# Performance work log

Hardware: AMD Instinct MI355X
Metric: run time of the kernel (lower is better)

The kernel has to match this reference:

```python
import jax, jax.numpy as jnp
import numpy as np

B, S, HID = 1, 4096, 2048
NH, NKV, D = 16, 4, 128
BLK, M, K_TOP = 64, 32, 8
THETA = 10000.0
NEG = jnp.float32(-1e9)


def setup_inputs() -> dict:
    key = jax.random.key(0)
    ks = jax.random.split(key, 6)
    s = 0.02
    return {
        "hidden_states": jax.random.normal(ks[0], (B, S, HID), jnp.float32),
        "position_ids": jnp.arange(S, dtype=jnp.int32)[None, :],
        "Wq": jax.random.normal(ks[1], (HID, NH * D), jnp.float32) * s,
        "Wk": jax.random.normal(ks[2], (HID, NKV * D), jnp.float32) * s,
        "Wv": jax.random.normal(ks[3], (HID, NKV * D), jnp.float32) * s,
        "Wo": jax.random.normal(ks[4], (NH * D, HID), jnp.float32) * s,
        # seeded random-sign (Hadamard-style) sketch projection, non-trainable buffer
        "H_sketch": jnp.sign(jax.random.normal(ks[5], (D, M), jnp.float32)) / jnp.sqrt(jnp.float32(M)),
    }


def _rot_half(x):
    x1, x2 = x[..., : D // 2], x[..., D // 2 :]
    return jnp.concatenate([-x2, x1], axis=-1)


def reference(hidden_states, position_ids, Wq, Wk, Wv, Wo, H_sketch):
    # QKV projections -> [B, heads, S, D]
    q = (hidden_states @ Wq).reshape(B, S, NH, D).transpose(0, 2, 1, 3)
    k = (hidden_states @ Wk).reshape(B, S, NKV, D).transpose(0, 2, 1, 3)
    v = (hidden_states @ Wv).reshape(B, S, NKV, D).transpose(0, 2, 1, 3)

    # RoPE
    inv_freq = 1.0 / (THETA ** (jnp.arange(0, D, 2, dtype=jnp.float32) / D))
    freqs = position_ids.astype(jnp.float32)[:, :, None] * inv_freq[None, None, :]
    emb = jnp.concatenate([freqs, freqs], axis=-1)  # [B, S, D]
    cos, sin = jnp.cos(emb)[:, None], jnp.sin(emb)[:, None]  # [B, 1, S, D]
    q = q * cos + _rot_half(q) * sin
    k = k * cos + _rot_half(k) * sin

    # GQA repeat kv heads
    rep = NH // NKV
    k = jnp.repeat(k, rep, axis=1)
    v = jnp.repeat(v, rep, axis=1)

    nblk = S // BLK
    # Hadamard-sketch projections, block-mean pooled -> [B, NH, nblk, M]
    Sq = jnp.einsum("bhsd,dm->bhsm", q, H_sketch).reshape(B, NH, nblk, BLK, M).mean(axis=3)
    Sk = jnp.einsum("bhsd,dm->bhsm", k, H_sketch).reshape(B, NH, nblk, BLK, M).mean(axis=3)

    # Block-level sketch scores, causal at block granularity, diagonal forced in
    bs = jnp.einsum("bhim,bhjm->bhij", Sq, Sk)
    blk_causal = jnp.tril(jnp.ones((nblk, nblk), dtype=bool))
    bs = jnp.where(blk_causal, bs, NEG)
    bs = jnp.where(jnp.eye(nblk, dtype=bool), jnp.float32(1e9), bs)
    _, idx = jax.lax.top_k(bs, K_TOP)  # [B, NH, nblk, K_TOP]

    # Gather selected K/V blocks -> [B, NH, nblk, K_TOP, BLK, D]
    K5 = k.reshape(B, NH, nblk, BLK, D)
    V5 = v.reshape(B, NH, nblk, BLK, D)
    gidx = idx[..., None, None]
    Kg = jnp.take_along_axis(K5[:, :, None], gidx, axis=3)
    Vg = jnp.take_along_axis(V5[:, :, None], gidx, axis=3)

    # Block-sparse scores [B, NH, nblk, BLK, K_TOP, BLK]
    Qb = q.reshape(B, NH, nblk, BLK, D)
    scores = jnp.einsum("bhnqd,bhnkcd->bhnqkc", Qb, Kg) / jnp.sqrt(jnp.float32(D))

    # Token-level causal mask over gathered keys
    qpos = jnp.arange(nblk)[:, None] * BLK + jnp.arange(BLK)[None, :]  # [nblk, BLK]
    kpos = idx[..., None] * BLK + jnp.arange(BLK)  # [B, NH, nblk, K_TOP, BLK]
    mask = kpos[:, :, :, None] <= qpos[None, None, :, :, None, None]
    scores = jnp.where(mask, scores, NEG)

    probs = jax.nn.softmax(scores.reshape(B, NH, nblk, BLK, K_TOP * BLK), axis=-1)
    probs = probs.reshape(scores.shape)

    out = jnp.einsum("bhnqkc,bhnkcd->bhnqd", probs, Vg)
    out = out.reshape(B, NH, S, D).transpose(0, 2, 1, 3).reshape(B, S, NH * D)
    return out @ Wo
```

## Files before the change

### kernel.cpp

```cpp
#include <hip/hip_runtime.h>
#include <hip/hip_bf16.h>

#define S_LEN 4096
#define HID 2048
#define NH 16
#define NKV 4
#define HD 128
#define MSK 32
#define KTOP 8
#define NBLK 64
#define NEGV -1000000000.0f
#define SENT -3.0e38f

typedef __hip_bfloat16 bf16;
typedef __attribute__((ext_vector_type(8))) short short8;
typedef __attribute__((ext_vector_type(4))) float f32x4;


__device__ __forceinline__ unsigned short f2b(float v) {
    __hip_bfloat16 h = __float2bfloat16(v);
    return *reinterpret_cast<unsigned short*>(&h);
}
__device__ __forceinline__ float b2f(unsigned short u) {
    return __bfloat162float(*reinterpret_cast<__hip_bfloat16*>(&u));
}

__global__ __launch_bounds__(256) void splitT_W(
    const float* __restrict__ Wq, const float* __restrict__ Wk,
    const float* __restrict__ Wv, const float* __restrict__ Wo,
    bf16* __restrict__ WtqH, bf16* __restrict__ WtqL,
    bf16* __restrict__ WtkH, bf16* __restrict__ WtkL,
    bf16* __restrict__ WtvH, bf16* __restrict__ WtoH) {
    const int bx = blockIdx.x, k0 = blockIdx.y * 64;
    const float* W; unsigned short* TH; unsigned short* TL;
    int Nd, n0; bool hasLo;
    if (bx < 32)      { W = Wq; TH = (unsigned short*)WtqH; TL = (unsigned short*)WtqL; Nd = 2048; n0 = bx * 64; hasLo = true; }
    else if (bx < 40) { W = Wk; TH = (unsigned short*)WtkH; TL = (unsigned short*)WtkL; Nd = 512;  n0 = (bx - 32) * 64; hasLo = true; }
    else if (bx < 48) { W = Wv; TH = (unsigned short*)WtvH; TL = nullptr; Nd = 512;  n0 = (bx - 40) * 64; hasLo = false; }
    else              { W = Wo; TH = (unsigned short*)WtoH; TL = nullptr; Nd = 2048; n0 = (bx - 48) * 64; hasLo = false; }
    __shared__ float Ls[64][68];
    const int t = threadIdx.x;
    {
        const int kk = t >> 2, c0 = (t & 3) * 16;
#pragma unroll
        for (int i = 0; i < 4; i++)
            *(float4*)&Ls[kk][c0 + i * 4] =
                *(const float4*)&W[(size_t)(k0 + kk) * Nd + n0 + c0 + i * 4];
    }
    __syncthreads();
    const int c = t >> 2, ks = (t & 3) * 16;
    alignas(16) unsigned short hh[16];
    alignas(16) unsigned short ll[16];
#pragma unroll
    for (int j = 0; j < 16; j++) {
        const float x = Ls[ks + j][c];
        hh[j] = f2b(x);
        ll[j] = f2b(x - b2f(hh[j]));
    }
    const size_t db = (size_t)(n0 + c) * HID + k0 + ks;
    *(uint4*)&TH[db + 0] = *(const uint4*)&hh[0];
    *(uint4*)&TH[db + 8] = *(const uint4*)&hh[8];
    if (hasLo) {
        *(uint4*)&TL[db + 0] = *(const uint4*)&ll[0];
        *(uint4*)&TL[db + 8] = *(const uint4*)&ll[8];
    }
}

__global__ __launch_bounds__(256) void splitA(const float* __restrict__ A,
                                              bf16* __restrict__ Ahi,
                                              bf16* __restrict__ Alo) {
    const size_t i = ((size_t)blockIdx.x * 256 + threadIdx.x) * 4;
    const float4 v = *(const float4*)&A[i];
    ushort4 h, l;
    h.x = f2b(v.x); l.x = f2b(v.x - b2f(h.x));
    h.y = f2b(v.y); l.y = f2b(v.y - b2f(h.y));
    h.z = f2b(v.z); l.z = f2b(v.z - b2f(h.z));
    h.w = f2b(v.w); l.w = f2b(v.w - b2f(h.w));
    *(ushort4*)&((unsigned short*)Ahi)[i] = h;
    *(ushort4*)&((unsigned short*)Alo)[i] = l;
}

__global__ __launch_bounds__(256, 3) void proj3(
    const float* __restrict__ A,
    const bf16* __restrict__ Ahi_, const bf16* __restrict__ Alo_,
    const bf16* __restrict__ WtqH_, const bf16* __restrict__ WtqL_,
    const bf16* __restrict__ WtkH_, const bf16* __restrict__ WtkL_,
    const bf16* __restrict__ WtvH_,
    const int* __restrict__ pos_ids, const float* __restrict__ H,
    bf16* __restrict__ qf, bf16* __restrict__ kf, bf16* __restrict__ vfT,
    float* __restrict__ Sq, float* __restrict__ Sk) {
    const int u = blockIdx.x;
    const bool isQ = (u < 16);
    const bool isV = (u >= 20);
    const bool np3 = !isV;
    const int h = isQ ? u : (isV ? (u - 20) : (u - 16));
    const unsigned short* __restrict__ WH =
        (const unsigned short*)(isQ ? WtqH_ : (isV ? WtvH_ : WtkH_)) + (size_t)h * HD * HID;
    const unsigned short* __restrict__ WL =
        (const unsigned short*)(isQ ? WtqL_ : WtkL_) + (size_t)h * HD * HID;
    const unsigned short* __restrict__ AH = (const unsigned short*)Ahi_;
    const unsigned short* __restrict__ AL = (const unsigned short*)Alo_;
    bf16* __restrict__ Xout = isQ ? qf : kf;
    float* __restrict__ Sout = isQ ? Sq : Sk;
    const int Nd = isQ ? (NH * HD) : (NKV * HD);

    const int m0g = blockIdx.y * 128;
    const int t = threadIdx.x;
    const int w = t >> 6, L = t & 63;
    const int lm = L & 15, lq = L >> 4;

    __shared__ __align__(16) unsigned short shmem[4 * 128 * 40];
    __shared__ float red[4][128];
    unsigned short(*pAh)[40] = (unsigned short(*)[40])(shmem);
    unsigned short(*pAl)[40] = (unsigned short(*)[40])(shmem + 128 * 40);
    unsigned short(*pWh)[40] = (unsigned short(*)[40])(shmem + 2 * 128 * 40);
    unsigned short(*pWl)[40] = (unsigned short(*)[40])(shmem + 3 * 128 * 40);

    f32x4 acc[2][8];
#pragma unroll
    for (int mt = 0; mt < 2; mt++)
#pragma unroll
        for (int nt = 0; nt < 8; nt++) acc[mt][nt] = (f32x4){0.f, 0.f, 0.f, 0.f};

    const int hrow = t >> 1, hk0 = (t & 1) * 16;

    for (int k0 = 0; k0 < HID; k0 += 32) {
        __syncthreads();
        if (AH) {
            const unsigned short* sa = &AH[(size_t)(m0g + hrow) * HID + k0 + hk0];
            *(uint4*)&pAh[hrow][hk0 + 0] = *(const uint4*)&sa[0];
            *(uint4*)&pAh[hrow][hk0 + 8] = *(const uint4*)&sa[8];
            if (np3) {
                const unsigned short* sl = &AL[(size_t)(m0g + hrow) * HID + k0 + hk0];
                *(uint4*)&pAl[hrow][hk0 + 0] = *(const uint4*)&sl[0];
                *(uint4*)&pAl[hrow][hk0 + 8] = *(const uint4*)&sl[8];
            }
        } else {
#pragma unroll
            for (int i = 0; i < 4; i++) {
                const int idx = t + i * 256;
                const int row = idx >> 3, f4 = idx & 7;
                const float4 v = *(const float4*)&A[(size_t)(m0g + row) * HID + k0 + f4 * 4];
                ushort4 uh;
                uh.x = f2b(v.x); uh.y = f2b(v.y); uh.z = f2b(v.z); uh.w = f2b(v.w);
                *(ushort4*)&pAh[row][f4 * 4] = uh;
                if (np3) {
                    ushort4 ul;
                    ul.x = f2b(v.x - b2f(uh.x)); ul.y = f2b(v.y - b2f(uh.y));
                    ul.z = f2b(v.z - b2f(uh.z)); ul.w = f2b(v.w - b2f(uh.w));
                    *(ushort4*)&pAl[row][f4 * 4] = ul;
                }
            }
        }
        {
            const unsigned short* sh = &WH[(size_t)hrow * HID + k0 + hk0];
            *(uint4*)&pWh[hrow][hk0 + 0] = *(const uint4*)&sh[0];
            *(uint4*)&pWh[hrow][hk0 + 8] = *(const uint4*)&sh[8];
            if (np3) {
                const unsigned short* sl = &WL[(size_t)hrow * HID + k0 + hk0];
                *(uint4*)&pWl[hrow][hk0 + 0] = *(const uint4*)&sl[0];
                *(uint4*)&pWl[hrow][hk0 + 8] = *(const uint4*)&sl[8];
            }
        }
        __syncthreads();
        short8 ah[2], al[2];
#pragma unroll
        for (int mt = 0; mt < 2; mt++) {
            ah[mt] = *(const short8*)&pAh[w * 32 + mt * 16 + lm][lq * 8];
            if (np3) al[mt] = *(const short8*)&pAl[w * 32 + mt * 16 + lm][lq * 8];
        }
#pragma unroll
        for (int nt = 0; nt < 8; nt++) {
            const short8 bh = *(const short8*)&pWh[nt * 16 + lm][lq * 8];
#pragma unroll
            for (int mt = 0; mt < 2; mt++)
                acc[mt][nt] = __builtin_amdgcn_mfma_f32_16x16x32_bf16(ah[mt], bh, acc[mt][nt], 0, 0, 0);
            if (np3) {
                const short8 bl = *(const short8*)&pWl[nt * 16 + lm][lq * 8];
#pragma unroll
                for (int mt = 0; mt < 2; mt++) {
                    acc[mt][nt] = __builtin_amdgcn_mfma_f32_16x16x32_bf16(ah[mt], bl, acc[mt][nt], 0, 0, 0);
                    acc[mt][nt] = __builtin_amdgcn_mfma_f32_16x16x32_bf16(al[mt], bh, acc[mt][nt], 0, 0, 0);
                }
            }
        }
    }

    if (isV) {
        __syncthreads();
        unsigned short(*Tv)[136] = (unsigned short(*)[136])shmem;
#pragma unroll
        for (int mt = 0; mt < 2; mt++) {
            const int rb = w * 32 + mt * 16 + lq * 4;
#pragma unroll
            for (int rr = 0; rr < 4; rr++)
#pragma unroll
                for (int nt = 0; nt < 8; nt++)
                    Tv[nt * 16 + lm][rb + rr] = f2b(acc[mt][nt][rr]);
        }
        __syncthreads();
        const int col = t >> 1, rh = (t & 1) * 64;
        bf16* dst = &vfT[((size_t)h * HD + col) * S_LEN + m0g + rh];
#pragma unroll
        for (int u2 = 0; u2 < 8; u2++)
            *(uint4*)&dst[u2 * 8] = *(const uint4*)&Tv[col][rh + u2 * 8];
        return;
    }

    {
        float invf[4];
#pragma unroll
        for (int c4 = 0; c4 < 4; c4++) {
            const int jj = c4 * 16 + lm;
            invf[c4] = 1.0f / powf(10000.0f, (float)jj * (1.0f / 64.0f));
        }
#pragma unroll
        for (int mt = 0; mt < 2; mt++) {
            const int rbase = w * 32 + mt * 16 + lq * 4;
#pragma unroll
            for (int rr = 0; rr < 4; rr++) {
                const float p = (float)pos_ids[m0g + rbase + rr];
#pragma unroll
                for (int c4 = 0; c4 < 4; c4++) {
                    const float fr = p * invf[c4];
                    float sv, cv;
                    sincosf(fr, &sv, &cv);
                    const float x1 = acc[mt][c4][rr];
                    const float x2 = acc[mt][c4 + 4][rr];
                    acc[mt][c4][rr]     = x1 * cv - x2 * sv;
                    acc[mt][c4 + 4][rr] = x2 * cv + x1 * sv;
                }
            }
        }
    }

    float cs[8];
#pragma unroll
    for (int nt = 0; nt < 8; nt++) cs[nt] = 0.f;
#pragma unroll
    for (int mt = 0; mt < 2; mt++) {
        const int rbase = w * 32 + mt * 16 + lq * 4;
#pragma unroll
        for (int rr = 0; rr < 4; rr++) {
            bf16* dst = &Xout[(size_t)(m0g + rbase + rr) * Nd + h * HD + lm];
#pragma unroll
            for (int nt = 0; nt < 8; nt++) {
                const float v = acc[mt][nt][rr];
                dst[nt * 16] = __float2bfloat16(v);
                cs[nt] += v;
            }
        }
    }
#pragma unroll
    for (int nt = 0; nt < 8; nt++) {
        cs[nt] += __shfl_xor(cs[nt], 16);
        cs[nt] += __shfl_xor(cs[nt], 32);
    }
    if (lq == 0) {
#pragma unroll
        for (int nt = 0; nt < 8; nt++) red[w][nt * 16 + lm] = cs[nt];
    }
    __syncthreads();
    if (t < 64) {
        const int b = t >> 5, m = t & 31;
        float s = 0.f;
        for (int d = 0; d < 128; d++)
            s += (red[b * 2][d] + red[b * 2 + 1][d]) * H[d * MSK + m];
        Sout[((size_t)h * NBLK + (m0g >> 6) + b) * MSK + m] = s * (1.0f / 64.0f);
    }
}

__global__ __launch_bounds__(256, 3) void proj_rope_sketch(
    const float* __restrict__ A, const float* __restrict__ Wq,
    const float* __restrict__ Wk, const float* __restrict__ Wv,
    const int* __restrict__ pos_ids, const float* __restrict__ H,
    bf16* __restrict__ qf, bf16* __restrict__ kf, bf16* __restrict__ vf,
    float* __restrict__ Sq, float* __restrict__ Sk,
    int u0, int r0, int xbase) {
    const int u = blockIdx.x + u0;
    const bool isQ = (u < 16);
    const bool isV = (u >= 20);
    const bool np3 = !isV;
    const int h = isQ ? u : (isV ? (u - 20) : (u - 16));
    const float* __restrict__ W = isQ ? Wq : (isV ? Wv : Wk);
    const int Nd = isQ ? (NH * HD) : (NKV * HD);
    bf16* __restrict__ Xout = isQ ? qf : kf;
    float* __restrict__ Sout = isQ ? Sq : Sk;

    const int m0g = r0 + blockIdx.y * 128;
    const int m0x = isQ ? (m0g - xbase) : m0g;
    const int t = threadIdx.x;
    const int w = t >> 6, L = t & 63;
    const int lm = L & 15, lq = L >> 4;

    __shared__ __align__(16) unsigned short shmem[4 * 128 * 40];
    __shared__ float red[4][128];
    unsigned short(*pAh)[40] = (unsigned short(*)[40])(shmem);
    unsigned short(*pAl)[40] = (unsigned short(*)[40])(shmem + 128 * 40);
    unsigned short(*pWh)[40] = (unsigned short(*)[40])(shmem + 2 * 128 * 40);
    unsigned short(*pWl)[40] = (unsigned short(*)[40])(shmem + 3 * 128 * 40);

    f32x4 acc[2][8];
#pragma unroll
    for (int mt = 0; mt < 2; mt++)
#pragma unroll
        for (int nt = 0; nt < 8; nt++) acc[mt][nt] = (f32x4){0.f, 0.f, 0.f, 0.f};

    for (int k0 = 0; k0 < HID; k0 += 32) {
        __syncthreads();
#pragma unroll
        for (int i = 0; i < 4; i++) {
            const int idx = t + i * 256;
            const int row = idx >> 3, f4 = idx & 7;
            const float4 v = *(const float4*)&A[(size_t)(m0g + row) * HID + k0 + f4 * 4];
            ushort4 uh;
            uh.x = f2b(v.x); uh.y = f2b(v.y); uh.z = f2b(v.z); uh.w = f2b(v.w);
            *(ushort4*)&pAh[row][f4 * 4] = uh;
            if (np3) {
                ushort4 ul;
                ul.x = f2b(v.x - b2f(uh.x)); ul.y = f2b(v.y - b2f(uh.y));
                ul.z = f2b(v.z - b2f(uh.z)); ul.w = f2b(v.w - b2f(uh.w));
                *(ushort4*)&pAl[row][f4 * 4] = ul;
            }
        }
        {
            const int wcol = t >> 1, wk0 = (t & 1) * 16;
            const float* wp = &W[(size_t)(k0 + wk0) * Nd + h * HD + wcol];
            alignas(16) unsigned short hh[16];
            alignas(16) unsigned short ll[16];
#pragma unroll
            for (int uu = 0; uu < 16; uu++) {
                const float x = wp[(size_t)uu * Nd];
                hh[uu] = f2b(x);
                ll[uu] = f2b(x - b2f(hh[uu]));
            }
            *(uint4*)&pWh[wcol][wk0 + 0] = *(const uint4*)&hh[0];
            *(uint4*)&pWh[wcol][wk0 + 8] = *(const uint4*)&hh[8];
            if (np3) {
                *(uint4*)&pWl[wcol][wk0 + 0] = *(const uint4*)&ll[0];
                *(uint4*)&pWl[wcol][wk0 + 8] = *(const uint4*)&ll[8];
            }
        }
        __syncthreads();
        short8 ah[2], al[2];
#pragma unroll
        for (int mt = 0; mt < 2; mt++) {
            ah[mt] = *(const short8*)&pAh[w * 32 + mt * 16 + lm][lq * 8];
            if (np3) al[mt] = *(const short8*)&pAl[w * 32 + mt * 16 + lm][lq * 8];
        }
#pragma unroll
        for (int nt = 0; nt < 8; nt++) {
            const short8 bh = *(const short8*)&pWh[nt * 16 + lm][lq * 8];
#pragma unroll
            for (int mt = 0; mt < 2; mt++)
                acc[mt][nt] = __builtin_amdgcn_mfma_f32_16x16x32_bf16(ah[mt], bh, acc[mt][nt], 0, 0, 0);
            if (np3) {
                const short8 bl = *(const short8*)&pWl[nt * 16 + lm][lq * 8];
#pragma unroll
                for (int mt = 0; mt < 2; mt++) {
                    acc[mt][nt] = __builtin_amdgcn_mfma_f32_16x16x32_bf16(ah[mt], bl, acc[mt][nt], 0, 0, 0);
                    acc[mt][nt] = __builtin_amdgcn_mfma_f32_16x16x32_bf16(al[mt], bh, acc[mt][nt], 0, 0, 0);
                }
            }
        }
    }

    if (isV) {
        __syncthreads();
        unsigned short(*Tv)[136] = (unsigned short(*)[136])shmem;
#pragma unroll
        for (int mt = 0; mt < 2; mt++) {
            const int rb = w * 32 + mt * 16 + lq * 4;
#pragma unroll
            for (int rr = 0; rr < 4; rr++)
#pragma unroll
                for (int nt = 0; nt < 8; nt++)
                    Tv[nt * 16 + lm][rb + rr] = f2b(acc[mt][nt][rr]);
        }
        __syncthreads();
        const int col = t >> 1, rh = (t & 1) * 64;
        bf16* dst = &vf[((size_t)h * HD + col) * S_LEN + m0g + rh];
#pragma unroll
        for (int u2 = 0; u2 < 8; u2++)
            *(uint4*)&dst[u2 * 8] = *(const uint4*)&Tv[col][rh + u2 * 8];
        return;
    }

    {
        float invf[4];
#pragma unroll
        for (int c4 = 0; c4 < 4; c4++) {
            const int jj = c4 * 16 + lm;
            invf[c4] = 1.0f / powf(10000.0f, (float)jj * (1.0f / 64.0f));
        }
#pragma unroll
        for (int mt = 0; mt < 2; mt++) {
            const int rbase = w * 32 + mt * 16 + lq * 4;
#pragma unroll
            for (int rr = 0; rr < 4; rr++) {
                const float p = (float)pos_ids[m0g + rbase + rr];
#pragma unroll
                for (int c4 = 0; c4 < 4; c4++) {
                    const float fr = p * invf[c4];
                    float sv, cv;
                    sincosf(fr, &sv, &cv);
                    const float x1 = acc[mt][c4][rr];
                    const float x2 = acc[mt][c4 + 4][rr];
                    acc[mt][c4][rr]     = x1 * cv - x2 * sv;
                    acc[mt][c4 + 4][rr] = x2 * cv + x1 * sv;
                }
            }
        }
    }

    float cs[8];
#pragma unroll
    for (int nt = 0; nt < 8; nt++) cs[nt] = 0.f;
#pragma unroll
    for (int mt = 0; mt < 2; mt++) {
        const int rbase = w * 32 + mt * 16 + lq * 4;
#pragma unroll
        for (int rr = 0; rr < 4; rr++) {
            bf16* dst = &Xout[(size_t)(m0x + rbase + rr) * Nd + h * HD + lm];
#pragma unroll
            for (int nt = 0; nt < 8; nt++) {
                const float v = acc[mt][nt][rr];
                dst[nt * 16] = __float2bfloat16(v);
                cs[nt] += v;
            }
        }
    }
#pragma unroll
    for (int nt = 0; nt < 8; nt++) {
        cs[nt] += __shfl_xor(cs[nt], 16);
        cs[nt] += __shfl_xor(cs[nt], 32);
    }
    if (lq == 0) {
#pragma unroll
        for (int nt = 0; nt < 8; nt++) red[w][nt * 16 + lm] = cs[nt];
    }
    __syncthreads();
    if (t < 64) {
        const int b = t >> 5, m = t & 31;
        float s = 0.f;
        for (int d = 0; d < 128; d++)
            s += (red[b * 2][d] + red[b * 2 + 1][d]) * H[d * MSK + m];
        Sout[((size_t)h * NBLK + (m0g >> 6) + b) * MSK + m] = s * (1.0f / 64.0f);
    }
}

__global__ __launch_bounds__(64) void topk_kernel(const float* __restrict__ Sq,
                                                  const float* __restrict__ Sk,
                                                  int* __restrict__ topk, int i0) {
    const int i = i0 + blockIdx.x, h = blockIdx.y, kv = h >> 2;
    const int j = threadIdx.x;
    __shared__ float vals[64];
    float v;
    if (j > i) v = NEGV;
    else if (j == i) v = 1e9f;
    else {
        v = 0.f;
        const float* sq = Sq + ((size_t)h * NBLK + i) * MSK;
        const float* sk = Sk + ((size_t)kv * NBLK + j) * MSK;
        for (int m = 0; m < MSK; m++) v += sq[m] * sk[m];
    }
    vals[j] = v;
    __syncthreads();
    if (j == 0) {
        for (int kk = 0; kk < KTOP; kk++) {
            float best = SENT; int bi = 0;
            for (int jj = 0; jj < 64; jj++)
                if (vals[jj] > best) { best = vals[jj]; bi = jj; }
            vals[bi] = SENT;
            topk[((size_t)h * NBLK + i) * KTOP + kk] = bi;
        }
    }
}

__global__ __launch_bounds__(256) void attn_kernel(bf16* __restrict__ qf,
                                                   const bf16* __restrict__ kf,
                                                   const bf16* __restrict__ vfT,
                                                   const int* __restrict__ topk,
                                                   int r0, int qbase) {
    const int qbg = (r0 >> 6) + blockIdx.x;
    const int h = blockIdx.y, kvh = h >> 2;
    const int t = threadIdx.x;
    const int w = t >> 6, L = t & 63;
    const int lm = L & 15, lq = L >> 4;

    __shared__ __align__(16) unsigned short Ks[64][136];
    __shared__ __align__(16) unsigned short Vt[128][72];
    __shared__ __align__(16) unsigned short Ps[64][72];

    short8 qfrag[4];
    {
        const size_t qrow = (size_t)(qbg * 64 - qbase) + w * 16 + lm;
        const unsigned short* qp = (const unsigned short*)qf + qrow * (NH * HD) + h * HD;
#pragma unroll
        for (int ks = 0; ks < 4; ks++)
            qfrag[ks] = *(const short8*)&qp[ks * 32 + lq * 8];
    }
    f32x4 O[8];
#pragma unroll
    for (int nt = 0; nt < 8; nt++) O[nt] = (f32x4){0.f, 0.f, 0.f, 0.f};
    f32x4 mrow = (f32x4){-1e30f, -1e30f, -1e30f, -1e30f};
    f32x4 lrow = (f32x4){0.f, 0.f, 0.f, 0.f};

    const int* sel = topk + ((size_t)h * NBLK + qbg) * KTOP;
    const int qpos0 = qbg * 64 + w * 16 + lq * 4;
    const float scale = 0.08838834764831845f;

    for (int kb = 0; kb < KTOP; kb++) {
        const int blk = sel[kb] & 63;
        __syncthreads();
#pragma unroll
        for (int i = 0; i < 4; i++) {
            const int idx = t + i * 256;
            const int rr = idx >> 4, c8 = idx & 15;
            *(uint4*)&Ks[rr][c8 * 8] =
                *(const uint4*)&kf[(size_t)(blk * 64 + rr) * (NKV * HD) + kvh * HD + c8 * 8];
        }
#pragma unroll
        for (int i = 0; i < 4; i++) {
            const int idx = t + i * 256;
            const int dd = idx >> 3, j8 = idx & 7;
            *(uint4*)&Vt[dd][j8 * 8] =
                *(const uint4*)&vfT[((size_t)kvh * HD + dd) * S_LEN + blk * 64 + j8 * 8];
        }
        __syncthreads();
        f32x4 S4[4];
#pragma unroll
        for (int nt = 0; nt < 4; nt++) {
            S4[nt] = (f32x4){0.f, 0.f, 0.f, 0.f};
#pragma unroll
            for (int ks = 0; ks < 4; ks++) {
                const short8 bk = *(const short8*)&Ks[nt * 16 + lm][ks * 32 + lq * 8];
                S4[nt] = __builtin_amdgcn_mfma_f32_16x16x32_bf16(qfrag[ks], bk, S4[nt], 0, 0, 0);
            }
        }
#pragma unroll
        for (int nt = 0; nt < 4; nt++) {
            const int kpos = blk * 64 + nt * 16 + lm;
#pragma unroll
            for (int r = 0; r < 4; r++)
                S4[nt][r] = (kpos <= qpos0 + r) ? S4[nt][r] * scale : NEGV;
        }
        f32x4 mx = S4[0];
#pragma unroll
        for (int nt = 1; nt < 4; nt++)
#pragma unroll
            for (int r = 0; r < 4; r++) mx[r] = fmaxf(mx[r], S4[nt][r]);
#pragma unroll
        for (int d = 1; d < 16; d <<= 1)
#pragma unroll
            for (int r = 0; r < 4; r++) mx[r] = fmaxf(mx[r], __shfl_xor(mx[r], d));
        f32x4 mnew, alv, sum;
#pragma unroll
        for (int r = 0; r < 4; r++) {
            mnew[r] = fmaxf(mrow[r], mx[r]);
            alv[r] = __expf(mrow[r] - mnew[r]);
            sum[r] = 0.f;
        }
#pragma unroll
        for (int nt = 0; nt < 4; nt++)
#pragma unroll
            for (int r = 0; r < 4; r++) {
                const float p = __expf(S4[nt][r] - mnew[r]);
                S4[nt][r] = p;
                sum[r] += p;
            }
#pragma unroll
        for (int d = 1; d < 16; d <<= 1)
#pragma unroll
            for (int r = 0; r < 4; r++) sum[r] += __shfl_xor(sum[r], d);
#pragma unroll
        for (int r = 0; r < 4; r++) {
            lrow[r] = lrow[r] * alv[r] + sum[r];
            mrow[r] = mnew[r];
        }
#pragma unroll
        for (int nt = 0; nt < 4; nt++)
#pragma unroll
            for (int r = 0; r < 4; r++)
                Ps[w * 16 + lq * 4 + r][nt * 16 + lm] = f2b(S4[nt][r]);
#pragma unroll
        for (int nt = 0; nt < 8; nt++)
#pragma unroll
            for (int r = 0; r < 4; r++) O[nt][r] *= alv[r];
#pragma unroll
        for (int ks2 = 0; ks2 < 2; ks2++) {
            const short8 pa = *(const short8*)&Ps[w * 16 + lm][ks2 * 32 + lq * 8];
#pragma unroll
            for (int nt = 0; nt < 8; nt++) {
                const short8 vv = *(const short8*)&Vt[nt * 16 + lm][ks2 * 32 + lq * 8];
                O[nt] = __builtin_amdgcn_mfma_f32_16x16x32_bf16(pa, vv, O[nt], 0, 0, 0);
            }
        }
    }
    f32x4 inv;
#pragma unroll
    for (int r = 0; r < 4; r++) inv[r] = 1.0f / lrow[r];
    const size_t orow0 = (size_t)(qbg * 64 - qbase) + w * 16 + lq * 4;
#pragma unroll
    for (int nt = 0; nt < 8; nt++)
#pragma unroll
        for (int r = 0; r < 4; r++)
            qf[(orow0 + r) * (NH * HD) + h * HD + nt * 16 + lm] =
                __float2bfloat16(O[nt][r] * inv[r]);
}

__global__ __launch_bounds__(256) void gemm_out(const bf16* __restrict__ A,
                                                const float* __restrict__ W,
                                                float* __restrict__ C, int cRow0) {
    __shared__ __align__(16) unsigned short Wl[128][40];
    const int n0 = blockIdx.x * 128, m0 = blockIdx.y * 128;
    const int t = threadIdx.x;
    const int w = t >> 6, L = t & 63;
    const int lm = L & 15, lq = L >> 4;
    const int wcol = t >> 1, wk0 = (t & 1) * 16;
    f32x4 acc[2][8];
#pragma unroll
    for (int mt = 0; mt < 2; mt++)
#pragma unroll
        for (int nt = 0; nt < 8; nt++) acc[mt][nt] = (f32x4){0.f, 0.f, 0.f, 0.f};

    float wreg[16];
    {
        const float* wp = &W[(size_t)wk0 * HID + n0 + wcol];
#pragma unroll
        for (int u = 0; u < 16; u++) wreg[u] = wp[(size_t)u * HID];
    }
    short8 av[2];
#pragma unroll
    for (int mt = 0; mt < 2; mt++)
        av[mt] = *(const short8*)&A[(size_t)(m0 + w * 32 + mt * 16 + lm) * HID + lq * 8];

    for (int k0 = 0; k0 < HID; k0 += 32) {
        __syncthreads();
        {
            alignas(16) unsigned short hh[16];
#pragma unroll
            for (int u = 0; u < 16; u++) hh[u] = f2b(wreg[u]);
            *(uint4*)&Wl[wcol][wk0 + 0] = *(const uint4*)&hh[0];
            *(uint4*)&Wl[wcol][wk0 + 8] = *(const uint4*)&hh[8];
        }
        const int k1 = k0 + 32;
        if (k1 < HID) {
            const float* wp = &W[(size_t)(k1 + wk0) * HID + n0 + wcol];
#pragma unroll
            for (int u = 0; u < 16; u++) wreg[u] = wp[(size_t)u * HID];
        }
        __syncthreads();
        short8 avn[2];
        if (k1 < HID) {
#pragma unroll
            for (int mt = 0; mt < 2; mt++)
                avn[mt] = *(const short8*)&A[(size_t)(m0 + w * 32 + mt * 16 + lm) * HID + k1 + lq * 8];
        }
#pragma unroll
        for (int nt = 0; nt < 8; nt++) {
            const short8 bv = *(const short8*)&Wl[nt * 16 + lm][lq * 8];
#pragma unroll
            for (int mt = 0; mt < 2; mt++)
                acc[mt][nt] = __builtin_amdgcn_mfma_f32_16x16x32_bf16(av[mt], bv, acc[mt][nt], 0, 0, 0);
        }
        if (k1 < HID) { av[0] = avn[0]; av[1] = avn[1]; }
    }
#pragma unroll
    for (int mt = 0; mt < 2; mt++)
#pragma unroll
        for (int nt = 0; nt < 8; nt++)
#pragma unroll
            for (int r = 0; r < 4; r++) {
                const int row = m0 + w * 32 + mt * 16 + lq * 4 + r;
                C[(size_t)(cRow0 + row) * HID + n0 + nt * 16 + lm] = acc[mt][nt][r];
            }
}

__global__ __launch_bounds__(256) void gemm_out2(const bf16* __restrict__ A,
                                                 const bf16* __restrict__ WtoH,
                                                 float* __restrict__ C) {
    __shared__ __align__(16) unsigned short Wl[128][72];
    const int n0 = blockIdx.x * 128, m0 = blockIdx.y * 128;
    const int t = threadIdx.x;
    const int w = t >> 6, L = t & 63;
    const int lm = L & 15, lq = L >> 4;
    const int ct = t >> 1, sg = (t & 1) * 32;
    const unsigned short* __restrict__ WT = (const unsigned short*)WtoH;
    f32x4 acc[2][8];
#pragma unroll
    for (int mt = 0; mt < 2; mt++)
#pragma unroll
        for (int nt = 0; nt < 8; nt++) acc[mt][nt] = (f32x4){0.f, 0.f, 0.f, 0.f};

    uint4 wbuf[4];
    {
        const unsigned short* wp = &WT[(size_t)(n0 + ct) * HID + sg];
#pragma unroll
        for (int i = 0; i < 4; i++) wbuf[i] = *(const uint4*)&wp[i * 8];
    }
    short8 av[2][2];
#pragma unroll
    for (int mt = 0; mt < 2; mt++)
#pragma unroll
        for (int ks = 0; ks < 2; ks++)
            av[mt][ks] = *(const short8*)&A[(size_t)(m0 + w * 32 + mt * 16 + lm) * HID + ks * 32 + lq * 8];

    for (int k0 = 0; k0 < HID; k0 += 64) {
        __syncthreads();
#pragma unroll
        for (int i = 0; i < 4; i++) *(uint4*)&Wl[ct][sg + i * 8] = wbuf[i];
        const int k1 = k0 + 64;
        if (k1 < HID) {
            const unsigned short* wp = &WT[(size_t)(n0 + ct) * HID + k1 + sg];
#pragma unroll
            for (int i = 0; i < 4; i++) wbuf[i] = *(const uint4*)&wp[i * 8];
        }
        __syncthreads();
        short8 avn[2][2];
        if (k1 < HID) {
#pragma unroll
            for (int mt = 0; mt < 2; mt++)
#pragma unroll
                for (int ks = 0; ks < 2; ks++)
                    avn[mt][ks] = *(const short8*)&A[(size_t)(m0 + w * 32 + mt * 16 + lm) * HID + k1 + ks * 32 + lq * 8];
        }
#pragma unroll
        for (int ks = 0; ks < 2; ks++)
#pragma unroll
            for (int nt = 0; nt < 8; nt++) {
                const short8 bv = *(const short8*)&Wl[nt * 16 + lm][ks * 32 + lq * 8];
#pragma unroll
                for (int mt = 0; mt < 2; mt++)
                    acc[mt][nt] = __builtin_amdgcn_mfma_f32_16x16x32_bf16(av[mt][ks], bv, acc[mt][nt], 0, 0, 0);
            }
        if (k1 < HID) {
#pragma unroll
            for (int mt = 0; mt < 2; mt++)
#pragma unroll
                for (int ks = 0; ks < 2; ks++) av[mt][ks] = avn[mt][ks];
        }
    }
#pragma unroll
    for (int mt = 0; mt < 2; mt++)
#pragma unroll
        for (int nt = 0; nt < 8; nt++)
#pragma unroll
            for (int r = 0; r < 4; r++) {
                const int row = m0 + w * 32 + mt * 16 + lq * 4 + r;
                C[(size_t)row * HID + n0 + nt * 16 + lm] = acc[mt][nt][r];
            }
}

extern "C" void kernel_launch(void* const* d_in, const int* in_sizes, int n_in,
                              void* d_out, int out_size, void* d_ws, size_t ws_size,
                              hipStream_t stream) {
    const void *p_hid, *p_pos, *p_wq, *p_wk, *p_wv, *p_wo, *p_h;
    if (in_sizes[0] == 4096 && in_sizes[1] == 1048576) {
        p_h = d_in[0]; p_wk = d_in[1]; p_wo = d_in[2]; p_wq = d_in[3];
        p_wv = d_in[4]; p_hid = d_in[5]; p_pos = d_in[6];
    } else {
        p_hid = d_in[0]; p_pos = d_in[1]; p_wq = d_in[2]; p_wk = d_in[3];
        p_wv = d_in[4]; p_wo = d_in[5]; p_h = d_in[6];
    }
    const float* hidden = (const float*)p_hid;
    const int* pos_ids  = (const int*)p_pos;
    const float* Wq = (const float*)p_wq;
    const float* Wk = (const float*)p_wk;
    const float* Wv = (const float*)p_wv;
    const float* Wo = (const float*)p_wo;
    const float* Hsk = (const float*)p_h;
    float* out = (float*)d_out;

    char* base = (char*)d_ws;
    float* Sq    = (float*)base;
    float* Sk    = (float*)(base + 131072);
    int*   topkb = (int*)(base + 163840);
    bf16*  kf    = (bf16*)(base + 196608);
    bf16*  vfT   = (bf16*)(base + 196608 + 4194304);
    bf16*  qbuf  = (bf16*)(base + 196608 + 8388608);
    bf16*  WtqH  = (bf16*)(base + 25362432);
    bf16*  WtqL  = (bf16*)(base + 33751040);
    bf16*  WtkH  = (bf16*)(base + 42139648);
    bf16*  WtkL  = (bf16*)(base + 44236800);
    bf16*  WtvH  = (bf16*)(base + 46333952);
    bf16*  WtoH  = (bf16*)(base + 48431104);
    bf16*  Ahi   = (bf16*)(base + 56819712);
    bf16*  Alo   = (bf16*)(base + 73596928);
    const size_t FULL_NEED  = 25362432;
    const size_t FULL2_NEED = 48431104;
    const size_t FULL3_NEED = 56819712;
    const size_t FULL4_NEED = 90374144;

    if (ws_size >= FULL2_NEED) {
        const bool hasWo = (ws_size >= FULL3_NEED);
        const bool hasA  = (ws_size >= FULL4_NEED);
        splitT_W<<<dim3(hasWo ? 80 : 48, 32), 256, 0, stream>>>(
            Wq, Wk, Wv, Wo, WtqH, WtqL, WtkH, WtkL, WtvH, WtoH);
        if (hasA)
            splitA<<<dim3((S_LEN * HID) / (256 * 4)), 256, 0, stream>>>(
                hidden, Ahi, Alo);
        proj3<<<dim3(24, 32), 256, 0, stream>>>(
            hidden, hasA ? Ahi : nullptr, hasA ? Alo : nullptr,
            WtqH, WtqL, WtkH, WtkL, WtvH, pos_ids, Hsk,
            qbuf, kf, vfT, Sq, Sk);
        topk_kernel<<<dim3(NBLK, NH), 64, 0, stream>>>(Sq, Sk, topkb, 0);
        attn_kernel<<<dim3(NBLK, NH), 256, 0, stream>>>(
            qbuf, kf, vfT, topkb, 0, 0);
        if (hasWo)
            gemm_out2<<<dim3(HID / 128, S_LEN / 128), 256, 0, stream>>>(
                qbuf, WtoH, out);
        else
            gemm_out<<<dim3(HID / 128, S_LEN / 128), 256, 0, stream>>>(
                qbuf, Wo, out, 0);
    } else if (ws_size >= FULL_NEED) {
        proj_rope_sketch<<<dim3(24, S_LEN / 128), 256, 0, stream>>>(
            hidden, Wq, Wk, Wv, pos_ids, Hsk, qbuf, kf, vfT, Sq, Sk, 0, 0, 0);
        topk_kernel<<<dim3(NBLK, NH), 64, 0, stream>>>(Sq, Sk, topkb, 0);
        attn_kernel<<<dim3(NBLK, NH), 256, 0, stream>>>(
            qbuf, kf, vfT, topkb, 0, 0);
        gemm_out<<<dim3(HID / 128, S_LEN / 128), 256, 0, stream>>>(
            qbuf, Wo, out, 0);
    } else {
        proj_rope_sketch<<<dim3(8, S_LEN / 128), 256, 0, stream>>>(
            hidden, Wq, Wk, Wv, pos_ids, Hsk, qbuf, kf, vfT, Sq, Sk, 16, 0, 0);
        for (int c = 0; c < 16; c++) {
            const int r0 = c * 256;
            proj_rope_sketch<<<dim3(16, 2), 256, 0, stream>>>(
                hidden, Wq, Wk, Wv, pos_ids, Hsk, qbuf, kf, vfT, Sq, Sk, 0, r0, r0);
            topk_kernel<<<dim3(4, NH), 64, 0, stream>>>(Sq, Sk, topkb, r0 >> 6);
            attn_kernel<<<dim3(4, NH), 256, 0, stream>>>(
                qbuf, kf, vfT, topkb, r0, r0);
            gemm_out<<<dim3(HID / 128, 2), 256, 0, stream>>>(
                qbuf, Wo, out, r0);
        }
    }
}
```

Before: 497.6 us.

## Pre-tile and swizzle split bf16 operands, load projection tiles via global_load_lds

The weight and activation split kernels now write hi/lo bf16 data into contiguous 8KB K-tiles with an XOR swizzle. This lets the projection GEMM stream each tile straight into LDS with 16-byte global_load_lds, bypassing registers. The LDS reads use the matching swizzle in place of padded rows to avoid bank conflicts. Wo is split by its own simpler kernel. The aim is to cut load-instruction overhead and LDS conflicts in the projection loop, at the cost of a more complex layout and still no double buffering.

```diff
diff --git a/kernel.cpp b/kernel.cpp
--- a/kernel.cpp
+++ b/kernel.cpp
@@ -24,20 +24,52 @@
 __device__ __forceinline__ float b2f(unsigned short u) {
     return __bfloat162float(*reinterpret_cast<__hip_bfloat16*>(&u));
 }
-
-__global__ __launch_bounds__(256) void splitT_W(
+__device__ __forceinline__ void gl16(const void* g, void* l) {
+    __builtin_amdgcn_global_load_lds(
+        (const __attribute__((address_space(1))) void*)g,
+        (__attribute__((address_space(3))) void*)l, 16, 0, 0);
+}
+
+__global__ __launch_bounds__(256) void splitW_tiles(
     const float* __restrict__ Wq, const float* __restrict__ Wk,
-    const float* __restrict__ Wv, const float* __restrict__ Wo,
+    const float* __restrict__ Wv,
     bf16* __restrict__ WtqH, bf16* __restrict__ WtqL,
     bf16* __restrict__ WtkH, bf16* __restrict__ WtkL,
-    bf16* __restrict__ WtvH, bf16* __restrict__ WtoH) {
-    const int bx = blockIdx.x, k0 = blockIdx.y * 64;
-    const float* W; unsigned short* TH; unsigned short* TL;
-    int Nd, n0; bool hasLo;
-    if (bx < 32)      { W = Wq; TH = (unsigned short*)WtqH; TL = (unsigned short*)WtqL; Nd = 2048; n0 = bx * 64; hasLo = true; }
-    else if (bx < 40) { W = Wk; TH = (unsigned short*)WtkH; TL = (unsigned short*)WtkL; Nd = 512;  n0 = (bx - 32) * 64; hasLo = true; }
-    else if (bx < 48) { W = Wv; TH = (unsigned short*)WtvH; TL = nullptr; Nd = 512;  n0 = (bx - 40) * 64; hasLo = false; }
-    else              { W = Wo; TH = (unsigned short*)WtoH; TL = nullptr; Nd = 2048; n0 = (bx - 48) * 64; hasLo = false; }
+    bf16* __restrict__ WtvH) {
+    const int u = blockIdx.x, kt = blockIdx.y, k0 = kt * 32;
+    const float* W; char* TH; char* TL; int Nd, n0; bool hasLo;
+    if (u < 16)      { W = Wq; TH = (char*)WtqH + (size_t)u * 524288;        TL = (char*)WtqL + (size_t)u * 524288; Nd = 2048; n0 = u * 128; hasLo = true; }
+    else if (u < 20) { W = Wk; TH = (char*)WtkH + (size_t)(u - 16) * 524288; TL = (char*)WtkL + (size_t)(u - 16) * 524288; Nd = 512; n0 = (u - 16) * 128; hasLo = true; }
+    else             { W = Wv; TH = (char*)WtvH + (size_t)(u - 20) * 524288; TL = nullptr; Nd = 512; n0 = (u - 20) * 128; hasLo = false; }
+    __shared__ float Lw[32][132];
+    const int t = threadIdx.x;
+#pragma unroll
+    for (int i = 0; i < 4; i++) {
+        const int task = t + i * 256;
+        const int k = task >> 5, c4 = task & 31;
+        *(float4*)&Lw[k][c4 * 4] = *(const float4*)&W[(size_t)(k0 + k) * Nd + n0 + c4 * 4];
+    }
+    __syncthreads();
+#pragma unroll
+    for (int i = 0; i < 2; i++) {
+        const int task = t + i * 256;
+        const int col = task >> 2, lq = task & 3;
+        alignas(16) unsigned short hh[8], lo[8];
+#pragma unroll
+        for (int j = 0; j < 8; j++) {
+            const float x = Lw[lq * 8 + j][col];
+            hh[j] = f2b(x);
+            lo[j] = f2b(x - b2f(hh[j]));
+        }
+        const size_t off = (size_t)kt * 8192 + (size_t)(((col * 4 + lq) ^ (col & 7))) * 16;
+        *(uint4*)(TH + off) = *(const uint4*)hh;
+        if (hasLo) *(uint4*)(TL + off) = *(const uint4*)lo;
+    }
+}
+
+__global__ __launch_bounds__(256) void splitT_Wo(const float* __restrict__ Wo,
+                                                 bf16* __restrict__ WtoH) {
+    const int n0 = blockIdx.x * 64, k0 = blockIdx.y * 64;
     __shared__ float Ls[64][68];
     const int t = threadIdx.x;
     {
@@ -45,44 +77,49 @@
 #pragma unroll
         for (int i = 0; i < 4; i++)
             *(float4*)&Ls[kk][c0 + i * 4] =
-                *(const float4*)&W[(size_t)(k0 + kk) * Nd + n0 + c0 + i * 4];
+                *(const float4*)&Wo[(size_t)(k0 + kk) * HID + n0 + c0 + i * 4];
     }
     __syncthreads();
     const int c = t >> 2, ks = (t & 3) * 16;
     alignas(16) unsigned short hh[16];
-    alignas(16) unsigned short ll[16];
-#pragma unroll
-    for (int j = 0; j < 16; j++) {
-        const float x = Ls[ks + j][c];
-        hh[j] = f2b(x);
-        ll[j] = f2b(x - b2f(hh[j]));
-    }
+#pragma unroll
+    for (int j = 0; j < 16; j++) hh[j] = f2b(Ls[ks + j][c]);
+    unsigned short* TH = (unsigned short*)WtoH;
     const size_t db = (size_t)(n0 + c) * HID + k0 + ks;
     *(uint4*)&TH[db + 0] = *(const uint4*)&hh[0];
     *(uint4*)&TH[db + 8] = *(const uint4*)&hh[8];
-    if (hasLo) {
-        *(uint4*)&TL[db + 0] = *(const uint4*)&ll[0];
-        *(uint4*)&TL[db + 8] = *(const uint4*)&ll[8];
-    }
-}
-
-__global__ __launch_bounds__(256) void splitA(const float* __restrict__ A,
-                                              bf16* __restrict__ Ahi,
-                                              bf16* __restrict__ Alo) {
-    const size_t i = ((size_t)blockIdx.x * 256 + threadIdx.x) * 4;
-    const float4 v = *(const float4*)&A[i];
-    ushort4 h, l;
-    h.x = f2b(v.x); l.x = f2b(v.x - b2f(h.x));
-    h.y = f2b(v.y); l.y = f2b(v.y - b2f(h.y));
-    h.z = f2b(v.z); l.z = f2b(v.z - b2f(h.z));
-    h.w = f2b(v.w); l.w = f2b(v.w - b2f(h.w));
-    *(ushort4*)&((unsigned short*)Ahi)[i] = h;
-    *(ushort4*)&((unsigned short*)Alo)[i] = l;
-}
-
-__global__ __launch_bounds__(256, 3) void proj3(
+}
+
+__global__ __launch_bounds__(256) void splitA_tiles(const float* __restrict__ A,
+                                                    bf16* __restrict__ AhiT,
+                                                    bf16* __restrict__ AloT) {
+    const int rb = blockIdx.x, kt = blockIdx.y;
+    const int t = threadIdx.x;
+    char* DH = (char*)AhiT + ((size_t)rb * 64 + kt) * 8192;
+    char* DL = (char*)AloT + ((size_t)rb * 64 + kt) * 8192;
+#pragma unroll
+    for (int i = 0; i < 2; i++) {
+        const int task = t + i * 256;
+        const int row = task >> 2, lq = task & 3;
+        const float* ap = &A[(size_t)(rb * 128 + row) * HID + kt * 32 + lq * 8];
+        const float4 v0 = *(const float4*)ap;
+        const float4 v1 = *(const float4*)(ap + 4);
+        const float f[8] = {v0.x, v0.y, v0.z, v0.w, v1.x, v1.y, v1.z, v1.w};
+        alignas(16) unsigned short hh[8], lo[8];
+#pragma unroll
+        for (int j = 0; j < 8; j++) {
+            hh[j] = f2b(f[j]);
+            lo[j] = f2b(f[j] - b2f(hh[j]));
+        }
+        const size_t off = (size_t)(((row * 4 + lq) ^ (row & 7))) * 16;
+        *(uint4*)(DH + off) = *(const uint4*)hh;
+        *(uint4*)(DL + off) = *(const uint4*)lo;
+    }
+}
+
+__global__ __launch_bounds__(256, 3) void proj4(
     const float* __restrict__ A,
-    const bf16* __restrict__ Ahi_, const bf16* __restrict__ Alo_,
+    const bf16* __restrict__ AhiT_, const bf16* __restrict__ AloT_,
     const bf16* __restrict__ WtqH_, const bf16* __restrict__ WtqL_,
     const bf16* __restrict__ WtkH_, const bf16* __restrict__ WtkL_,
     const bf16* __restrict__ WtvH_,
@@ -94,27 +131,26 @@
     const bool isV = (u >= 20);
     const bool np3 = !isV;
     const int h = isQ ? u : (isV ? (u - 20) : (u - 16));
-    const unsigned short* __restrict__ WH =
-        (const unsigned short*)(isQ ? WtqH_ : (isV ? WtvH_ : WtkH_)) + (size_t)h * HD * HID;
-    const unsigned short* __restrict__ WL =
-        (const unsigned short*)(isQ ? WtqL_ : WtkL_) + (size_t)h * HD * HID;
-    const unsigned short* __restrict__ AH = (const unsigned short*)Ahi_;
-    const unsigned short* __restrict__ AL = (const unsigned short*)Alo_;
+    const char* WHb = (const char*)(isQ ? WtqH_ : (isV ? WtvH_ : WtkH_)) + (size_t)h * 524288;
+    const char* WLb = (const char*)(isQ ? WtqL_ : WtkL_) + (size_t)h * 524288;
+    const char* AHb = (const char*)AhiT_;
+    const char* ALb = (const char*)AloT_;
     bf16* __restrict__ Xout = isQ ? qf : kf;
     float* __restrict__ Sout = isQ ? Sq : Sk;
     const int Nd = isQ ? (NH * HD) : (NKV * HD);
 
-    const int m0g = blockIdx.y * 128;
+    const int rb = blockIdx.y;
+    const int m0g = rb * 128;
     const int t = threadIdx.x;
     const int w = t >> 6, L = t & 63;
     const int lm = L & 15, lq = L >> 4;
 
-    __shared__ __align__(16) unsigned short shmem[4 * 128 * 40];
+    __shared__ __align__(16) char arena[34816];
     __shared__ float red[4][128];
-    unsigned short(*pAh)[40] = (unsigned short(*)[40])(shmem);
-    unsigned short(*pAl)[40] = (unsigned short(*)[40])(shmem + 128 * 40);
-    unsigned short(*pWh)[40] = (unsigned short(*)[40])(shmem + 2 * 128 * 40);
-    unsigned short(*pWl)[40] = (unsigned short(*)[40])(shmem + 3 * 128 * 40);
+    char* Wh_s = arena;
+    char* Wl_s = arena + 8192;
+    char* Ah_s = arena + 16384;
+    char* Al_s = arena + 24576;
 
     f32x4 acc[2][8];
 #pragma unroll
@@ -122,61 +158,64 @@
 #pragma unroll
         for (int nt = 0; nt < 8; nt++) acc[mt][nt] = (f32x4){0.f, 0.f, 0.f, 0.f};
 
-    const int hrow = t >> 1, hk0 = (t & 1) * 16;
-
-    for (int k0 = 0; k0 < HID; k0 += 32) {
-        __syncthreads();
-        if (AH) {
-            const unsigned short* sa = &AH[(size_t)(m0g + hrow) * HID + k0 + hk0];
-            *(uint4*)&pAh[hrow][hk0 + 0] = *(const uint4*)&sa[0];
-            *(uint4*)&pAh[hrow][hk0 + 8] = *(const uint4*)&sa[8];
-            if (np3) {
-                const unsigned short* sl = &AL[(size_t)(m0g + hrow) * HID + k0 + hk0];
-                *(uint4*)&pAl[hrow][hk0 + 0] = *(const uint4*)&sl[0];
-                *(uint4*)&pAl[hrow][hk0 + 8] = *(const uint4*)&sl[8];
+    for (int kt = 0; kt < 64; kt++) {
+        __syncthreads();
+        const size_t tW = (size_t)kt * 8192;
+#pragma unroll
+        for (int i = 0; i < 2; i++) {
+            const int so = (w * 2 + i) * 1024;
+            gl16(WHb + tW + so + L * 16, Wh_s + so);
+            if (np3) gl16(WLb + tW + so + L * 16, Wl_s + so);
+        }
+        if (AHb) {
+            const size_t tA = ((size_t)rb * 64 + kt) * 8192;
+#pragma unroll
+            for (int i = 0; i < 2; i++) {
+                const int so = (w * 2 + i) * 1024;
+                gl16(AHb + tA + so + L * 16, Ah_s + so);
+                if (np3) gl16(ALb + tA + so + L * 16, Al_s + so);
             }
         } else {
-#pragma unroll
-            for (int i = 0; i < 4; i++) {
-                const int idx = t + i * 256;
-                const int row = idx >> 3, f4 = idx & 7;
-                const float4 v = *(const float4*)&A[(size_t)(m0g + row) * HID + k0 + f4 * 4];
-                ushort4 uh;
-                uh.x = f2b(v.x); uh.y = f2b(v.y); uh.z = f2b(v.z); uh.w = f2b(v.w);
-                *(ushort4*)&pAh[row][f4 * 4] = uh;
-                if (np3) {
-                    ushort4 ul;
-                    ul.x = f2b(v.x - b2f(uh.x)); ul.y = f2b(v.y - b2f(uh.y));
-                    ul.z = f2b(v.z - b2f(uh.z)); ul.w = f2b(v.w - b2f(uh.w));
-                    *(ushort4*)&pAl[row][f4 * 4] = ul;
+            const int k0 = kt * 32;
+#pragma unroll
+            for (int i = 0; i < 2; i++) {
+                const int task = t + i * 256;
+                const int row = task >> 2, q2 = task & 3;
+                const float* ap = &A[(size_t)(m0g + row) * HID + k0 + q2 * 8];
+                const float4 v0 = *(const float4*)ap;
+                const float4 v1 = *(const float4*)(ap + 4);
+                const float f[8] = {v0.x, v0.y, v0.z, v0.w, v1.x, v1.y, v1.z, v1.w};
+                alignas(16) unsigned short hh[8], lo[8];
+#pragma unroll
+                for (int j = 0; j < 8; j++) {
+                    hh[j] = f2b(f[j]);
+                    if (np3) lo[j] = f2b(f[j] - b2f(hh[j]));
                 }
-            }
-        }
-        {
-            const unsigned short* sh = &WH[(size_t)hrow * HID + k0 + hk0];
-            *(uint4*)&pWh[hrow][hk0 + 0] = *(const uint4*)&sh[0];
-            *(uint4*)&pWh[hrow][hk0 + 8] = *(const uint4*)&sh[8];
-            if (np3) {
-                const unsigned short* sl = &WL[(size_t)hrow * HID + k0 + hk0];
-                *(uint4*)&pWl[hrow][hk0 + 0] = *(const uint4*)&sl[0];
-                *(uint4*)&pWl[hrow][hk0 + 8] = *(const uint4*)&sl[8];
-            }
-        }
-        __syncthreads();
+                const int ch = ((row * 4 + q2) ^ (row & 7)) * 16;
+                *(uint4*)(Ah_s + ch) = *(const uint4*)hh;
+                if (np3) *(uint4*)(Al_s + ch) = *(const uint4*)lo;
+            }
+        }
+        __syncthreads();
+        const int xr = lm & 7;
         short8 ah[2], al[2];
 #pragma unroll
         for (int mt = 0; mt < 2; mt++) {
-            ah[mt] = *(const short8*)&pAh[w * 32 + mt * 16 + lm][lq * 8];
-            if (np3) al[mt] = *(const short8*)&pAl[w * 32 + mt * 16 + lm][lq * 8];
+            const int rowA = w * 32 + mt * 16 + lm;
+            const int cA = (((rowA * 4 + lq) ^ xr)) * 16;
+            ah[mt] = *(const short8*)(Ah_s + cA);
+            if (np3) al[mt] = *(const short8*)(Al_s + cA);
         }
 #pragma unroll
         for (int nt = 0; nt < 8; nt++) {
-            const short8 bh = *(const short8*)&pWh[nt * 16 + lm][lq * 8];
+            const int rowW = nt * 16 + lm;
+            const int cW = (((rowW * 4 + lq) ^ xr)) * 16;
+            const short8 bh = *(const short8*)(Wh_s + cW);
 #pragma unroll
             for (int mt = 0; mt < 2; mt++)
                 acc[mt][nt] = __builtin_amdgcn_mfma_f32_16x16x32_bf16(ah[mt], bh, acc[mt][nt], 0, 0, 0);
             if (np3) {
-                const short8 bl = *(const short8*)&pWl[nt * 16 + lm][lq * 8];
+                const short8 bl = *(const short8*)(Wl_s + cW);
 #pragma unroll
                 for (int mt = 0; mt < 2; mt++) {
                     acc[mt][nt] = __builtin_amdgcn_mfma_f32_16x16x32_bf16(ah[mt], bl, acc[mt][nt], 0, 0, 0);
@@ -188,15 +227,15 @@
 
     if (isV) {
         __syncthreads();
-        unsigned short(*Tv)[136] = (unsigned short(*)[136])shmem;
+        unsigned short(*Tv)[136] = (unsigned short(*)[136])arena;
 #pragma unroll
         for (int mt = 0; mt < 2; mt++) {
-            const int rb = w * 32 + mt * 16 + lq * 4;
+            const int rbs = w * 32 + mt * 16 + lq * 4;
 #pragma unroll
             for (int rr = 0; rr < 4; rr++)
 #pragma unroll
                 for (int nt = 0; nt < 8; nt++)
-                    Tv[nt * 16 + lm][rb + rr] = f2b(acc[mt][nt][rr]);
+                    Tv[nt * 16 + lm][rbs + rr] = f2b(acc[mt][nt][rr]);
         }
         __syncthreads();
         const int col = t >> 1, rh = (t & 1) * 64;
@@ -370,12 +409,12 @@
         unsigned short(*Tv)[136] = (unsigned short(*)[136])shmem;
 #pragma unroll
         for (int mt = 0; mt < 2; mt++) {
-            const int rb = w * 32 + mt * 16 + lq * 4;
+            const int rbs = w * 32 + mt * 16 + lq * 4;
 #pragma unroll
             for (int rr = 0; rr < 4; rr++)
 #pragma unroll
                 for (int nt = 0; nt < 8; nt++)
-                    Tv[nt * 16 + lm][rb + rr] = f2b(acc[mt][nt][rr]);
+                    Tv[nt * 16 + lm][rbs + rr] = f2b(acc[mt][nt][rr]);
         }
         __syncthreads();
         const int col = t >> 1, rh = (t & 1) * 64;
@@ -785,8 +824,8 @@
     bf16*  WtkL  = (bf16*)(base + 44236800);
     bf16*  WtvH  = (bf16*)(base + 46333952);
     bf16*  WtoH  = (bf16*)(base + 48431104);
-    bf16*  Ahi   = (bf16*)(base + 56819712);
-    bf16*  Alo   = (bf16*)(base + 73596928);
+    bf16*  AhiT  = (bf16*)(base + 56819712);
+    bf16*  AloT  = (bf16*)(base + 73596928);
     const size_t FULL_NEED  = 25362432;
     const size_t FULL2_NEED = 48431104;
     const size_t FULL3_NEED = 56819712;
@@ -795,13 +834,14 @@
     if (ws_size >= FULL2_NEED) {
         const bool hasWo = (ws_size >= FULL3_NEED);
         const bool hasA  = (ws_size >= FULL4_NEED);
-        splitT_W<<<dim3(hasWo ? 80 : 48, 32), 256, 0, stream>>>(
-            Wq, Wk, Wv, Wo, WtqH, WtqL, WtkH, WtkL, WtvH, WtoH);
+        splitW_tiles<<<dim3(24, 64), 256, 0, stream>>>(
+            Wq, Wk, Wv, WtqH, WtqL, WtkH, WtkL, WtvH);
+        if (hasWo)
+            splitT_Wo<<<dim3(32, 32), 256, 0, stream>>>(Wo, WtoH);
         if (hasA)
-            splitA<<<dim3((S_LEN * HID) / (256 * 4)), 256, 0, stream>>>(
-                hidden, Ahi, Alo);
-        proj3<<<dim3(24, 32), 256, 0, stream>>>(
-            hidden, hasA ? Ahi : nullptr, hasA ? Alo : nullptr,
+            splitA_tiles<<<dim3(32, 64), 256, 0, stream>>>(hidden, AhiT, AloT);
+        proj4<<<dim3(24, 32), 256, 0, stream>>>(
+            hidden, hasA ? AhiT : nullptr, hasA ? AloT : nullptr,
             WtqH, WtqL, WtkH, WtkL, WtvH, pos_ids, Hsk,
             qbuf, kf, vfT, Sq, Sk);
         topk_kernel<<<dim3(NBLK, NH), 64, 0, stream>>>(Sq, Sk, topkb, 0);
```

After: 460.9 us. 7.4% less time.
